# Kernel optimization log

Hardware: AMD Instinct MI355X
Metric: run time of the kernel (lower is better)

Reference implementation:

```python
import jax, jax.numpy as jnp
import numpy as np
from jax import lax

C_IN = 256
P = 4
S_D = 512
N_GROUPS = C_IN // P          # 64
C_OUT = C_IN                  # 256
CIN_G = C_IN // N_GROUPS      # 4 (in-channels per group, depthwise stage)
COUT_G = C_OUT // N_GROUPS    # 4 (channels per group, pointwise stage)
EPS = 1e-5


def setup_inputs() -> dict:
    key = jax.random.key(0)
    ks = jax.random.split(key, 8)
    style_encoding = jax.random.normal(ks[0], (8, S_D, 4, 4), dtype=jnp.float32)
    predicted = jax.random.normal(ks[1], (8, C_IN, 128, 128), dtype=jnp.float32)
    # kernel-generator parameters (xavier-ish scale)
    dw_w = jax.random.normal(ks[2], (C_OUT * CIN_G, S_D, 2, 2), dtype=jnp.float32) * 0.03
    dw_b = jnp.full((C_OUT * CIN_G,), 0.01, dtype=jnp.float32)
    pw_kn_w = jax.random.normal(ks[3], (C_OUT * COUT_G, S_D, 1, 1), dtype=jnp.float32) * 0.05
    pw_kn_b = jnp.full((C_OUT * COUT_G,), 0.01, dtype=jnp.float32)
    pw_b_w = jax.random.normal(ks[4], (C_OUT, S_D, 1, 1), dtype=jnp.float32) * 0.05
    pw_b_b = jnp.full((C_OUT,), 0.01, dtype=jnp.float32)
    return {"style_encoding": style_encoding, "predicted": predicted,
            "dw_w": dw_w, "dw_b": dw_b, "pw_kn_w": pw_kn_w, "pw_kn_b": pw_kn_b,
            "pw_b_w": pw_b_w, "pw_b_b": pw_b_b}


def reference(style_encoding, predicted, dw_w, dw_b, pw_kn_w, pw_kn_b, pw_b_w, pw_b_b):
    N = style_encoding.shape[0]
    # --- generate per-sample depthwise 3x3 grouped-conv kernels ---
    dw = lax.conv_general_dilated(style_encoding, dw_w, (1, 1), 'VALID',
                                  dimension_numbers=('NCHW', 'OIHW', 'NCHW'))
    dw = dw + dw_b[None, :, None, None]                 # [N, C_OUT*CIN_G, 3, 3]
    dw = dw.reshape(N, C_OUT, CIN_G, 3, 3)
    # --- double 2x2 avg pool on 4x4 style == global spatial mean ---
    s = jnp.mean(style_encoding, axis=(2, 3))           # [N, S_D]
    # 1x1 convs on 1x1 maps == linear layers
    pw_kn = (s @ pw_kn_w.reshape(C_OUT * COUT_G, S_D).T + pw_kn_b)
    pw_kn = pw_kn.reshape(N, N_GROUPS, COUT_G, COUT_G)  # [N, g, out/g, in/g]
    pw_bias = s @ pw_b_w.reshape(C_OUT, S_D).T + pw_b_b  # [N, C_OUT]
    # --- instance norm (no affine) on content features ---
    mean = predicted.mean(axis=(2, 3), keepdims=True)
    x = predicted - mean
    x = x * lax.rsqrt(jnp.mean(jnp.square(x), axis=(2, 3), keepdims=True) + EPS)
    # --- reflection pad (1,1,1,1) ---
    x = jnp.pad(x, ((0, 0), (0, 0), (1, 1), (1, 1)), mode='reflect')
    # --- per-sample grouped 3x3 conv, vectorized over batch via vmap ---
    def conv_one(xi, wi):
        return lax.conv_general_dilated(xi[None], wi, (1, 1), 'VALID',
                                        dimension_numbers=('NCHW', 'OIHW', 'NCHW'),
                                        feature_group_count=N_GROUPS)[0]
    y = jax.vmap(conv_one)(x, dw)                       # [N, C_OUT, H, W]
    # --- per-sample grouped 1x1 conv as a batched group einsum ---
    H, W = y.shape[2], y.shape[3]
    yg = y.reshape(N, N_GROUPS, COUT_G, H, W)
    out = jnp.einsum('ngihw,ngoi->ngohw', yg, pw_kn).reshape(N, C_OUT, H, W)
    out = out + pw_bias[:, :, None, None]
    return out
```

## Files before the change

kernel.cpp:

```cpp
#include <hip/hip_runtime.h>

#define NB 8
#define SD 512
#define HW 128
#define EPS 1e-5f

__device__ __forceinline__ int refl(int r) { return r < 0 ? 1 : (r > 127 ? 126 : r); }

__device__ __forceinline__ void async_copy16(const float* g, float* l) {
    __builtin_amdgcn_global_load_lds(
        (const __attribute__((address_space(1))) void*)g,
        (__attribute__((address_space(3))) void*)l, 16, 0, 0);
}

__global__ __launch_bounds__(256) void prep_k(const float* __restrict__ pred,
                                              const float* __restrict__ style,
                                              const float* __restrict__ dww,
                                              const float* __restrict__ dwb,
                                              float* __restrict__ s_ws,
                                              float* __restrict__ dw_ws,
                                              float* __restrict__ mean_ws,
                                              float* __restrict__ inv_ws) {
    __shared__ float ws4[4], wss4[4];
    int b = blockIdx.x, t = threadIdx.x;
    if (b < 2048) {
        const float4* p = (const float4*)(pred + (size_t)b * HW * HW);
        float s = 0.f, ss = 0.f;
#pragma unroll
        for (int k = 0; k < 16; ++k) {
            float4 v = p[k * 256 + t];
            s  += v.x + v.y + v.z + v.w;
            ss += v.x * v.x + v.y * v.y + v.z * v.z + v.w * v.w;
        }
#pragma unroll
        for (int off = 32; off; off >>= 1) {
            s  += __shfl_down(s, off);
            ss += __shfl_down(ss, off);
        }
        if ((t & 63) == 0) { ws4[t >> 6] = s; wss4[t >> 6] = ss; }
        __syncthreads();
        if (t == 0) {
            float S  = ws4[0] + ws4[1] + ws4[2] + ws4[3];
            float SS = wss4[0] + wss4[1] + wss4[2] + wss4[3];
            float m = S * (1.f / (HW * HW));
            float var = SS * (1.f / (HW * HW)) - m * m;
            mean_ws[b] = m;
            inv_ws[b] = rsqrtf(var + EPS);
        }
    } else if (b < 2064) {
        int u = (b - 2048) * 256 + t;
        const float* p = style + (size_t)u * 16;
        float a = 0.f;
#pragma unroll
        for (int k = 0; k < 16; ++k) a += p[k];
        s_ws[u] = a * (1.f / 16.f);
    } else {
        int bb = b - 2064;
        int n = bb & 7;
        int f = ((bb >> 3) << 2) + (t >> 6);
        int lane = t & 63;
        float acc[9];
#pragma unroll
        for (int k = 0; k < 9; ++k) acc[k] = 0.f;
#pragma unroll 2
        for (int it = 0; it < 8; ++it) {
            int c = lane + (it << 6);
            const float4* sp = (const float4*)(style + ((size_t)n * SD + c) * 16);
            float st[16];
#pragma unroll
            for (int k = 0; k < 4; ++k) {
                float4 v = sp[k];
                st[k * 4 + 0] = v.x; st[k * 4 + 1] = v.y;
                st[k * 4 + 2] = v.z; st[k * 4 + 3] = v.w;
            }
            float4 w = *(const float4*)(dww + ((size_t)f * SD + c) * 4);
#pragma unroll
            for (int p = 0; p < 3; ++p)
#pragma unroll
                for (int q = 0; q < 3; ++q)
                    acc[p * 3 + q] += st[p * 4 + q] * w.x + st[p * 4 + q + 1] * w.y
                                    + st[(p + 1) * 4 + q] * w.z + st[(p + 1) * 4 + q + 1] * w.w;
        }
#pragma unroll
        for (int k = 0; k < 9; ++k)
#pragma unroll
            for (int off = 32; off; off >>= 1) acc[k] += __shfl_down(acc[k], off);
        if (lane == 0) {
            float bias = dwb[f];
#pragma unroll
            for (int k = 0; k < 9; ++k)
                dw_ws[((size_t)n * 1024 + f) * 9 + k] = acc[k] + bias;
        }
    }
}

__global__ __launch_bounds__(256) void gen_pw_k(const float* __restrict__ s_ws,
                                                const float* __restrict__ pkw,
                                                const float* __restrict__ pkb,
                                                const float* __restrict__ pbw,
                                                const float* __restrict__ pbb,
                                                float* __restrict__ pwk,
                                                float* __restrict__ pwbias) {
    int w = blockIdx.x * 4 + (threadIdx.x >> 6);
    int lane = threadIdx.x & 63;
    int n = w / 1280;
    int j = w - n * 1280;
    bool isk = j < 1024;
    const float2* wrow = (const float2*)(isk ? (pkw + (size_t)j * SD)
                                             : (pbw + (size_t)(j - 1024) * SD));
    const float2* s2 = (const float2*)(s_ws + (size_t)n * SD);
    float a = 0.f;
#pragma unroll
    for (int it = 0; it < 4; ++it) {
        int c2 = lane + (it << 6);
        float2 x = s2[c2];
        float2 v = wrow[c2];
        a += x.x * v.x + x.y * v.y;
    }
#pragma unroll
    for (int off = 32; off; off >>= 1) a += __shfl_down(a, off);
    if (lane == 0) {
        if (isk) pwk[(size_t)n * 1024 + j] = a + pkb[j];
        else     pwbias[(size_t)n * 256 + (j - 1024)] = a + pbb[j - 1024];
    }
}

__global__ __launch_bounds__(192) void fold_k(float* __restrict__ dw_ws,
                                              const float* __restrict__ pwk_ws,
                                              float* __restrict__ pwb_ws,
                                              const float* __restrict__ mean_ws,
                                              const float* __restrict__ inv_ws) {
    __shared__ float dwl[144], pwkl[16], invl[4], msc[4], pwbl[4];
    int b = blockIdx.x;
    int n = b >> 6, g = b & 63;
    int t = threadIdx.x;
    size_t dbase = (size_t)(n * 1024 + g * 16) * 9;
    if (t < 144) dwl[t] = dw_ws[dbase + t];
    else if (t < 160) pwkl[t - 144] = pwk_ws[(size_t)n * 1024 + g * 16 + (t - 144)];
    else if (t < 164) {
        int ic = t - 160;
        float m = mean_ws[n * 256 + g * 4 + ic];
        float s = inv_ws[n * 256 + g * 4 + ic];
        invl[ic] = s; msc[ic] = m * s;
    } else if (t < 168) {
        pwbl[t - 164] = pwb_ws[n * 256 + g * 4 + (t - 164)];
    }
    __syncthreads();
    if (t < 144) {
        int o = t / 36, rm = t % 36, ic = rm / 9, k = rm % 9;
        int kh = k / 3, kw = k % 3;
        float a = 0.f;
#pragma unroll
        for (int i = 0; i < 4; ++i) a += pwkl[o * 4 + i] * dwl[(i * 4 + ic) * 9 + k];
        dw_ws[dbase + (size_t)(((ic * 3 + kh) * 3 + kw) * 4 + o)] = a * invl[ic];
    } else if (t < 148) {
        int o = t - 144;
        float cb = 0.f;
#pragma unroll
        for (int i = 0; i < 4; ++i) {
            float s2 = 0.f;
#pragma unroll
            for (int ic = 0; ic < 4; ++ic) {
                float sk = 0.f;
#pragma unroll
                for (int k = 0; k < 9; ++k) sk += dwl[(i * 4 + ic) * 9 + k];
                s2 += msc[ic] * sk;
            }
            cb += pwkl[o * 4 + i] * s2;
        }
        pwb_ws[n * 256 + g * 4 + o] = pwbl[o] - cb;
    }
}

__global__ __launch_bounds__(256) void adaconv_main_k(const float* __restrict__ pred,
                                                      const float* __restrict__ Wf,
                                                      const float* __restrict__ Bf,
                                                      float* __restrict__ out) {
    __shared__ float tile[4][10][128];
    __shared__ float wf[148];
    int b = blockIdx.x;
    int strip = b & 15;
    int g = (b >> 4) & 63;
    int n = b >> 10;
    int t = threadIdx.x;
    const size_t gbase = (size_t)(n * 64 + g);
    const size_t cbase = (size_t)(n * 256 + g * 4);
    int r0 = strip << 3;

    {
        int wv = t >> 6, l = t & 63;
        const float* pc = pred + (cbase + wv) * (HW * HW) + ((l & 31) << 2);
        int rhalf = l >> 5;
#pragma unroll
        for (int rp = 0; rp < 5; ++rp) {
            int rr = refl(r0 - 1 + rp * 2 + rhalf);
            async_copy16(pc + rr * HW, &tile[wv][rp * 2][0]);
        }
    }

    if (t < 144) wf[t] = Wf[gbase * 144 + t];
    else if (t < 148) wf[t] = Bf[gbase * 4 + (t - 144)];

    __syncthreads();

    int row = t >> 5;
    int colq = t & 31;
    int qL = colq == 0 ? 0 : colq - 1;
    int qR = colq == 31 ? 31 : colq + 1;
    float acc[4][4];
#pragma unroll
    for (int o = 0; o < 4; ++o) {
        float bb = wf[144 + o];
#pragma unroll
        for (int p = 0; p < 4; ++p) acc[o][p] = bb;
    }

#pragma unroll
    for (int ic = 0; ic < 4; ++ic) {
#pragma unroll
        for (int kh = 0; kh < 3; ++kh) {
            const float4* rq = (const float4*)&tile[ic][row + kh][0];
            float4 v  = rq[colq];
            float4 vL = rq[qL];
            float4 vR = rq[qR];
            float e0 = (colq == 0)  ? v.y : vL.w;
            float e5 = (colq == 31) ? v.z : vR.x;
            float e[6] = {e0, v.x, v.y, v.z, v.w, e5};
            const float* wp = &wf[(ic * 3 + kh) * 12];
#pragma unroll
            for (int kw = 0; kw < 3; ++kw) {
                float4 wk = *(const float4*)(wp + kw * 4);
#pragma unroll
                for (int p = 0; p < 4; ++p) {
                    acc[0][p] = fmaf(wk.x, e[p + kw], acc[0][p]);
                    acc[1][p] = fmaf(wk.y, e[p + kw], acc[1][p]);
                    acc[2][p] = fmaf(wk.z, e[p + kw], acc[2][p]);
                    acc[3][p] = fmaf(wk.w, e[p + kw], acc[3][p]);
                }
            }
        }
    }

#pragma unroll
    for (int o = 0; o < 4; ++o) {
        *(float4*)(out + (cbase + o) * (HW * HW) + (size_t)(r0 + row) * HW + (colq << 2)) =
            make_float4(acc[o][0], acc[o][1], acc[o][2], acc[o][3]);
    }
}

extern "C" void kernel_launch(void* const* d_in, const int* in_sizes, int n_in,
                              void* d_out, int out_size, void* d_ws, size_t ws_size,
                              hipStream_t stream) {
    const float* style = (const float*)d_in[0];
    const float* pred  = (const float*)d_in[1];
    const float* dww   = (const float*)d_in[2];
    const float* dwb   = (const float*)d_in[3];
    const float* pkw   = (const float*)d_in[4];
    const float* pkb   = (const float*)d_in[5];
    const float* pbw   = (const float*)d_in[6];
    const float* pbb   = (const float*)d_in[7];
    float* out = (float*)d_out;

    float* ws      = (float*)d_ws;
    float* s_ws    = ws;
    float* dw_ws   = ws + 4096;
    float* pwk_ws  = ws + 77824;
    float* pwb_ws  = ws + 86016;
    float* mean_ws = ws + 88064;
    float* inv_ws  = ws + 90112;

    prep_k<<<4112, 256, 0, stream>>>(pred, style, dww, dwb, s_ws, dw_ws, mean_ws, inv_ws);
    gen_pw_k<<<2560, 256, 0, stream>>>(s_ws, pkw, pkb, pbw, pbb, pwk_ws, pwb_ws);
    fold_k<<<NB * 64, 192, 0, stream>>>(dw_ws, pwk_ws, pwb_ws, mean_ws, inv_ws);
    adaconv_main_k<<<8192, 256, 0, stream>>>(pred, dw_ws, pwb_ws, out);
}
```

Baseline: 102.7 us.

## Fuse style mean and pointwise kernel generation into fold kernel; nontemporal output stores

```diff
diff --git a/kernel.cpp b/kernel.cpp
--- a/kernel.cpp
+++ b/kernel.cpp
@@ -5,6 +5,8 @@
 #define HW 128
 #define EPS 1e-5f
 
+typedef float vf4 __attribute__((ext_vector_type(4)));
+
 __device__ __forceinline__ int refl(int r) { return r < 0 ? 1 : (r > 127 ? 126 : r); }
 
 __device__ __forceinline__ void async_copy16(const float* g, float* l) {
@@ -17,7 +19,6 @@
                                               const float* __restrict__ style,
                                               const float* __restrict__ dww,
                                               const float* __restrict__ dwb,
-                                              float* __restrict__ s_ws,
                                               float* __restrict__ dw_ws,
                                               float* __restrict__ mean_ws,
                                               float* __restrict__ inv_ws) {
@@ -47,15 +48,8 @@
             mean_ws[b] = m;
             inv_ws[b] = rsqrtf(var + EPS);
         }
-    } else if (b < 2064) {
-        int u = (b - 2048) * 256 + t;
-        const float* p = style + (size_t)u * 16;
-        float a = 0.f;
-#pragma unroll
-        for (int k = 0; k < 16; ++k) a += p[k];
-        s_ws[u] = a * (1.f / 16.f);
     } else {
-        int bb = b - 2064;
+        int bb = b - 2048;
         int n = bb & 7;
         int f = ((bb >> 3) << 2) + (t >> 6);
         int lane = t & 63;
@@ -94,58 +88,64 @@
     }
 }
 
-__global__ __launch_bounds__(256) void gen_pw_k(const float* __restrict__ s_ws,
-                                                const float* __restrict__ pkw,
-                                                const float* __restrict__ pkb,
-                                                const float* __restrict__ pbw,
-                                                const float* __restrict__ pbb,
-                                                float* __restrict__ pwk,
-                                                float* __restrict__ pwbias) {
-    int w = blockIdx.x * 4 + (threadIdx.x >> 6);
-    int lane = threadIdx.x & 63;
-    int n = w / 1280;
-    int j = w - n * 1280;
-    bool isk = j < 1024;
-    const float2* wrow = (const float2*)(isk ? (pkw + (size_t)j * SD)
-                                             : (pbw + (size_t)(j - 1024) * SD));
-    const float2* s2 = (const float2*)(s_ws + (size_t)n * SD);
-    float a = 0.f;
-#pragma unroll
-    for (int it = 0; it < 4; ++it) {
-        int c2 = lane + (it << 6);
-        float2 x = s2[c2];
-        float2 v = wrow[c2];
-        a += x.x * v.x + x.y * v.y;
-    }
-#pragma unroll
-    for (int off = 32; off; off >>= 1) a += __shfl_down(a, off);
-    if (lane == 0) {
-        if (isk) pwk[(size_t)n * 1024 + j] = a + pkb[j];
-        else     pwbias[(size_t)n * 256 + (j - 1024)] = a + pbb[j - 1024];
-    }
-}
-
-__global__ __launch_bounds__(192) void fold_k(float* __restrict__ dw_ws,
-                                              const float* __restrict__ pwk_ws,
-                                              float* __restrict__ pwb_ws,
-                                              const float* __restrict__ mean_ws,
-                                              const float* __restrict__ inv_ws) {
+__global__ __launch_bounds__(256) void fold2_k(const float* __restrict__ style,
+                                               const float* __restrict__ pkw,
+                                               const float* __restrict__ pkb,
+                                               const float* __restrict__ pbw,
+                                               const float* __restrict__ pbb,
+                                               const float* __restrict__ mean_ws,
+                                               const float* __restrict__ inv_ws,
+                                               float* __restrict__ dw_ws,
+                                               float* __restrict__ pwb_ws) {
+    __shared__ float s_lds[SD];
     __shared__ float dwl[144], pwkl[16], invl[4], msc[4], pwbl[4];
     int b = blockIdx.x;
     int n = b >> 6, g = b & 63;
     int t = threadIdx.x;
-    size_t dbase = (size_t)(n * 1024 + g * 16) * 9;
+    size_t dbase = (size_t)(n * 64 + g) * 144;
+
     if (t < 144) dwl[t] = dw_ws[dbase + t];
-    else if (t < 160) pwkl[t - 144] = pwk_ws[(size_t)n * 1024 + g * 16 + (t - 144)];
-    else if (t < 164) {
-        int ic = t - 160;
+    else if (t < 148) {
+        int ic = t - 144;
         float m = mean_ws[n * 256 + g * 4 + ic];
         float s = inv_ws[n * 256 + g * 4 + ic];
         invl[ic] = s; msc[ic] = m * s;
-    } else if (t < 168) {
-        pwbl[t - 164] = pwb_ws[n * 256 + g * 4 + (t - 164)];
+    }
+#pragma unroll
+    for (int c0 = 0; c0 < 2; ++c0) {
+        int c = t + (c0 << 8);
+        const float4* sp = (const float4*)(style + ((size_t)n * SD + c) * 16);
+        float4 a0 = sp[0], a1 = sp[1], a2 = sp[2], a3 = sp[3];
+        float sum = a0.x + a0.y + a0.z + a0.w + a1.x + a1.y + a1.z + a1.w
+                  + a2.x + a2.y + a2.z + a2.w + a3.x + a3.y + a3.z + a3.w;
+        s_lds[c] = sum * (1.f / 16.f);
     }
     __syncthreads();
+
+    int wv = t >> 6, lane = t & 63;
+#pragma unroll
+    for (int q = 0; q < 5; ++q) {
+        int u = wv * 5 + q;
+        const float2* wrow = (const float2*)((u < 16)
+                              ? (pkw + (size_t)(g * 16 + u) * SD)
+                              : (pbw + (size_t)(g * 4 + (u - 16)) * SD));
+        float a = 0.f;
+#pragma unroll
+        for (int it = 0; it < 4; ++it) {
+            int c2 = lane + (it << 6);
+            float2 x = ((const float2*)s_lds)[c2];
+            float2 v = wrow[c2];
+            a += x.x * v.x + x.y * v.y;
+        }
+#pragma unroll
+        for (int off = 32; off; off >>= 1) a += __shfl_down(a, off);
+        if (lane == 0) {
+            if (u < 16) pwkl[u] = a + pkb[g * 16 + u];
+            else        pwbl[u - 16] = a + pbb[g * 4 + (u - 16)];
+        }
+    }
+    __syncthreads();
+
     if (t < 144) {
         int o = t / 36, rm = t % 36, ic = rm / 9, k = rm % 9;
         int kh = k / 3, kw = k % 3;
@@ -243,8 +243,9 @@
 
 #pragma unroll
     for (int o = 0; o < 4; ++o) {
-        *(float4*)(out + (cbase + o) * (HW * HW) + (size_t)(r0 + row) * HW + (colq << 2)) =
-            make_float4(acc[o][0], acc[o][1], acc[o][2], acc[o][3]);
+        vf4 vv = {acc[o][0], acc[o][1], acc[o][2], acc[o][3]};
+        __builtin_nontemporal_store(vv,
+            (vf4*)(out + (cbase + o) * (HW * HW) + (size_t)(r0 + row) * HW + (colq << 2)));
     }
 }
 
@@ -262,15 +263,13 @@
     float* out = (float*)d_out;
 
     float* ws      = (float*)d_ws;
-    float* s_ws    = ws;
     float* dw_ws   = ws + 4096;
-    float* pwk_ws  = ws + 77824;
     float* pwb_ws  = ws + 86016;
     float* mean_ws = ws + 88064;
     float* inv_ws  = ws + 90112;
 
-    prep_k<<<4112, 256, 0, stream>>>(pred, style, dww, dwb, s_ws, dw_ws, mean_ws, inv_ws);
-    gen_pw_k<<<2560, 256, 0, stream>>>(s_ws, pkw, pkb, pbw, pbb, pwk_ws, pwb_ws);
-    fold_k<<<NB * 64, 192, 0, stream>>>(dw_ws, pwk_ws, pwb_ws, mean_ws, inv_ws);
+    prep_k<<<4096, 256, 0, stream>>>(pred, style, dww, dwb, dw_ws, mean_ws, inv_ws);
+    fold2_k<<<NB * 64, 256, 0, stream>>>(style, pkw, pkb, pbw, pbb,
+                                         mean_ws, inv_ws, dw_ws, pwb_ws);
     adaconv_main_k<<<8192, 256, 0, stream>>>(pred, dw_ws, pwb_ws, out);
 }
```

Result: slower. 147.7 us (+43.9%).
